# Kernel optimization log

Measured on AMD Instinct MI355X. Metric: run time of the kernel, lower is better.

The kernel has to match this reference:

```python
import jax, jax.numpy as jnp
import numpy as np

N_HEAD = 16
DROP_P = 0.1


def setup_inputs() -> dict:
    key = jax.random.key(0)
    ks = jax.random.split(key, 5)
    B, T, C = 2, 2048, 1024
    return {
        "x": jax.random.normal(ks[0], (B, T, C), dtype=jnp.float32),
        "w_attn": jax.random.normal(ks[1], (C, 3 * C), dtype=jnp.float32) * 0.02,
        "b_attn": jax.random.normal(ks[2], (3 * C,), dtype=jnp.float32) * 0.02,
        "w_proj": jax.random.normal(ks[3], (C, C), dtype=jnp.float32) * 0.02,
        "b_proj": jax.random.normal(ks[4], (C,), dtype=jnp.float32) * 0.02,
    }


def reference(x, w_attn, b_attn, w_proj, b_proj):
    B, T, C = x.shape
    H = N_HEAD
    D = C // H  # head dim
    qkv = x @ w_attn + b_attn                      # [B,T,3C]
    q, k, v = jnp.split(qkv, 3, axis=-1)
    # [B,T,C] -> [B,H,T,D]
    q = q.reshape(B, T, H, D).transpose(0, 2, 1, 3)
    k = k.reshape(B, T, H, D).transpose(0, 2, 1, 3)
    v = v.reshape(B, T, H, D).transpose(0, 2, 1, 3)
    scale = 1.0 / jnp.sqrt(jnp.float32(D))
    attn = jnp.einsum("bhqd,bhkd->bhqk", q, k) * scale  # [B,H,T,T]
    causal = jnp.tril(jnp.ones((T, T), dtype=bool))
    attn = jnp.where(causal[None, None], attn, jnp.float32(-jnp.inf))
    attn = jax.nn.softmax(attn, axis=-1)
    # dropout p=0.1 (training mode in original); deterministic fixed key here
    keep = jax.random.bernoulli(jax.random.key(42), 1.0 - DROP_P, attn.shape)
    attn = jnp.where(keep, attn / (1.0 - DROP_P), 0.0)
    out = jnp.einsum("bhqk,bhkd->bhqd", attn, v)   # [B,H,T,D]
    out = out.transpose(0, 2, 1, 3).reshape(B, T, C)
    return out @ w_proj + b_proj
```

## Files before the change

### kernel.cpp

```cpp
#include <hip/hip_runtime.h>
#include <hip/hip_bf16.h>
#include <stdint.h>
#include <math.h>

#define TSEQ   2048
#define NBATCH 2
#define NHEAD  16
#define HDIM   64
#define CDIM   1024

#define KEEP_LIMIT 3865470464u
#define QSC 0.18033688011112042f

typedef short  bf16x8 __attribute__((ext_vector_type(8)));
typedef float  f32x4  __attribute__((ext_vector_type(4)));

__device__ __forceinline__ float fast_exp2(float x) {
    float r; asm("v_exp_f32 %0, %1" : "=v"(r) : "v"(x)); return r;
}
__device__ __forceinline__ uint32_t cvt_pk_bf16(float a, float b) {
    uint32_t r; asm("v_cvt_pk_bf16_f32 %0, %1, %2" : "=v"(r) : "v"(a), "v"(b)); return r;
}

__device__ __forceinline__ uint32_t rotl32(uint32_t x, int r) {
    return __builtin_amdgcn_alignbit(x, x, 32 - r);
}

__device__ __forceinline__ uint32_t tf2x32_xor(uint32_t x0, uint32_t x1) {
    const uint32_t ka = 0u, kb = 42u;
    const uint32_t kc = ka ^ kb ^ 0x1BD11BDAu;
    x0 += ka; x1 += kb;
#define TFR(r) { x0 += x1; x1 = rotl32(x1, r); x1 ^= x0; }
    TFR(13) TFR(15) TFR(26) TFR(6)
    x0 += kb; x1 += kc + 1u;
    TFR(17) TFR(29) TFR(16) TFR(24)
    x0 += kc; x1 += ka + 2u;
    TFR(13) TFR(15) TFR(26) TFR(6)
    x0 += ka; x1 += kb + 3u;
    TFR(17) TFR(29) TFR(16) TFR(24)
    x0 += kb; x1 += kc + 4u;
    TFR(13) TFR(15) TFR(26) TFR(6)
    x0 += kc; x1 += ka + 5u;
#undef TFR
    return x0 ^ x1;
}

__device__ __forceinline__ float bf2f(ushort u) {
    union { uint32_t i; float f; } c; c.i = ((uint32_t)u) << 16; return c.f;
}

__device__ __forceinline__ void async_copy16(void* lds, const void* g) {
    __builtin_amdgcn_global_load_lds(
        (const __attribute__((address_space(1))) unsigned int*)g,
        (__attribute__((address_space(3))) unsigned int*)lds, 16, 0, 0);
}

__global__ __launch_bounds__(256) void prep(
    const float* __restrict__ x, ushort* __restrict__ xb,
    const float* __restrict__ wA, ushort* __restrict__ wTa,
    const float* __restrict__ wP, ushort* __restrict__ wTp)
{
    __shared__ float t[32][33];
    const int nb = blockIdx.x;
    const int i = threadIdx.x;
    if (nb < 2048) {
        int idx = (nb * 256 + i) * 8;
        float4 a = *(const float4*)(x + idx);
        float4 b = *(const float4*)(x + idx + 4);
        uint4 o;
        o.x = cvt_pk_bf16(a.x, a.y); o.y = cvt_pk_bf16(a.z, a.w);
        o.z = cvt_pk_bf16(b.x, b.y); o.w = cvt_pk_bf16(b.z, b.w);
        *(uint4*)(xb + idx) = o;
        return;
    }
    const float* src; ushort* dst; int n0, k0, N, K;
    if (nb < 5120) {
        int tt = nb - 2048;  src = wA; dst = wTa;
        n0 = (tt % 96) * 32; k0 = (tt / 96) * 32; N = 3072; K = 1024;
    } else {
        int tt = nb - 5120;  src = wP; dst = wTp;
        n0 = (tt & 31) * 32; k0 = (tt >> 5) * 32; N = 1024; K = 1024;
    }
    {
        int k = i >> 3, n4 = (i & 7) * 4;
        float4 v = *(const float4*)(src + (size_t)(k0 + k) * N + n0 + n4);
        t[k][n4 + 0] = v.x; t[k][n4 + 1] = v.y; t[k][n4 + 2] = v.z; t[k][n4 + 3] = v.w;
    }
    __syncthreads();
    {
        int n = i >> 3, k4 = (i & 7) * 4;
        uint2 o;
        o.x = cvt_pk_bf16(t[k4 + 0][n], t[k4 + 1][n]);
        o.y = cvt_pk_bf16(t[k4 + 2][n], t[k4 + 3][n]);
        *(uint2*)(dst + (size_t)(n0 + n) * K + k0 + k4) = o;
    }
}

__global__ __launch_bounds__(256) void qkv_mask(
    const ushort* __restrict__ A, const ushort* __restrict__ Bt,
    const float* __restrict__ bias,
    ushort* __restrict__ Q, ushort* __restrict__ Kq, ushort* __restrict__ V,
    unsigned long long* __restrict__ mask)
{
    __shared__ ushort As[2][128 * 32];
    __shared__ ushort Bs[2][128 * 32];
    const int tid = threadIdx.x, lane = tid & 63, wid = tid >> 6;

    if (blockIdx.x >= 768) {
        const int mb   = blockIdx.x - 768;
        const int hb   = mb >> 6;
        const int rem  = mb & 63;
        const int pair = rem >> 2;
        const int quad = rem & 3;
        const int lim  = (pair + 1) << 6;
        const int base = quad * 528 + wid * 132;
#pragma unroll 1
        for (int it = 0; it < 33; ++it) {
            uint32_t idxs[4], qrow[4]; int kts[4];
#pragma unroll
            for (int j = 0; j < 4; ++j) {
                const int u = base + it * 4 + j;
                const bool first = (u < lim);
                const int qt = first ? pair : 31 - pair;
                const int uu = first ? u : u - lim;
                const int kt = uu >> 6, q = uu & 63;
                qrow[j] = ((uint32_t)hb << 11) + (uint32_t)((qt << 6) + q);
                idxs[j] = qrow[j] * 2048u + (uint32_t)(kt << 6) + (uint32_t)lane;
                kts[j] = kt;
            }
            uint32_t bits[4];
#pragma unroll
            for (int j = 0; j < 4; ++j) bits[j] = tf2x32_xor(0u, idxs[j]);
#pragma unroll
            for (int j = 0; j < 4; ++j) {
                const unsigned long long bal = __ballot(bits[j] < KEEP_LIMIT);
                if (lane == j)
                    mask[((size_t)qrow[j] << 5) + kts[j]] = bal;
            }
        }
        return;
    }

    const int l15 = lane & 15, l4 = lane >> 4;
    const int wr = wid >> 1, wc = wid & 1;
    const int bn = blockIdx.x % 24, bm = blockIdx.x / 24;
    const int K = 1024, NTK = K >> 5;

    f32x4 acc[4][4];
#pragma unroll
    for (int m = 0; m < 4; ++m)
#pragma unroll
        for (int n = 0; n < 4; ++n) acc[m][n] = (f32x4){0.f, 0.f, 0.f, 0.f};

    auto stage = [&](int p, int k0) {
#pragma unroll
        for (int j = 0; j < 2; ++j) {
            const int rbase = wid * 32 + j * 16;
            const int row = rbase + (lane >> 2);
            const ushort* src = A + (size_t)(bm * 128 + row) * K + k0 + (lane & 3) * 8;
            async_copy16(&As[p][rbase * 32], src);
        }
#pragma unroll
        for (int j = 0; j < 2; ++j) {
            const int rbase = wid * 32 + j * 16;
            const int row = rbase + (lane >> 2);
            const ushort* src = Bt + (size_t)(bn * 128 + row) * K + k0 + (lane & 3) * 8;
            async_copy16(&Bs[p][rbase * 32], src);
        }
    };
    auto compute = [&](int p) {
        bf16x8 af[4], bf[4];
#pragma unroll
        for (int m = 0; m < 4; ++m)
            af[m] = *(const bf16x8*)&As[p][(wr * 64 + m * 16 + l15) * 32 + l4 * 8];
#pragma unroll
        for (int n = 0; n < 4; ++n)
            bf[n] = *(const bf16x8*)&Bs[p][(wc * 64 + n * 16 + l15) * 32 + l4 * 8];
#pragma unroll
        for (int m = 0; m < 4; ++m)
#pragma unroll
            for (int n = 0; n < 4; ++n)
                acc[m][n] = __builtin_amdgcn_mfma_f32_16x16x32_bf16(af[m], bf[n], acc[m][n], 0, 0, 0);
    };

    stage(0, 0);
    __syncthreads();
    for (int t = 0; t < NTK; ++t) {
        const int p = t & 1;
        if (t + 1 < NTK) stage(p ^ 1, (t + 1) << 5);
        compute(p);
        __syncthreads();
    }

    const int colbase = bn * 128 + wc * 64;
    const int rowbase = bm * 128 + wr * 64;
#pragma unroll
    for (int n = 0; n < 4; ++n) {
        const int col = colbase + n * 16 + l15;
        const int which = col >> 10, cc = col & 1023;
        const int hh = cc >> 6, dd = cc & 63;
        const float bv = bias[col];
        const float sc = (which == 0) ? QSC : 1.0f;
#pragma unroll
        for (int m = 0; m < 4; ++m) {
            float v0 = (acc[m][n][0] + bv) * sc, v1 = (acc[m][n][1] + bv) * sc;
            float v2 = (acc[m][n][2] + bv) * sc, v3 = (acc[m][n][3] + bv) * sc;
            uint32_t pk01 = cvt_pk_bf16(v0, v1), pk23 = cvt_pk_bf16(v2, v3);
            ushort vals[4] = { (ushort)pk01, (ushort)(pk01 >> 16),
                               (ushort)pk23, (ushort)(pk23 >> 16) };
#pragma unroll
            for (int r = 0; r < 4; ++r) {
                const int row = rowbase + m * 16 + l4 * 4 + r;
                const int bb = row >> 11, tt = row & 2047;
                if (which == 0)
                    Q[(((size_t)(bb * NHEAD + hh)) * TSEQ + tt) * HDIM + dd] = vals[r];
                else if (which == 1)
                    Kq[(((size_t)(bb * NHEAD + hh)) * TSEQ + tt) * HDIM + dd] = vals[r];
                else
                    V[(((size_t)(bb * NHEAD + hh)) * HDIM + dd) * TSEQ + tt] = vals[r];
            }
        }
    }
}

__global__ __launch_bounds__(256) void proj_gemm(
    const ushort* __restrict__ A, const ushort* __restrict__ Bt,
    const float* __restrict__ bias, float* __restrict__ Cf, int M, int N, int K)
{
    __shared__ ushort As[2][128 * 32];
    __shared__ ushort Bs[2][128 * 32];
    const int tid = threadIdx.x, lane = tid & 63, wid = tid >> 6;
    const int l15 = lane & 15, l4 = lane >> 4;
    const int wr = wid >> 1, wc = wid & 1;
    const int bn = blockIdx.x, bm = blockIdx.y;
    const int NTK = K >> 5;

    f32x4 acc[4][4];
#pragma unroll
    for (int m = 0; m < 4; ++m)
#pragma unroll
        for (int n = 0; n < 4; ++n) acc[m][n] = (f32x4){0.f, 0.f, 0.f, 0.f};

    auto stage = [&](int p, int k0) {
#pragma unroll
        for (int j = 0; j < 2; ++j) {
            const int rbase = wid * 32 + j * 16;
            const int row = rbase + (lane >> 2);
            const ushort* src = A + (size_t)(bm * 128 + row) * K + k0 + (lane & 3) * 8;
            async_copy16(&As[p][rbase * 32], src);
        }
#pragma unroll
        for (int j = 0; j < 2; ++j) {
            const int rbase = wid * 32 + j * 16;
            const int row = rbase + (lane >> 2);
            const ushort* src = Bt + (size_t)(bn * 128 + row) * K + k0 + (lane & 3) * 8;
            async_copy16(&Bs[p][rbase * 32], src);
        }
    };
    auto compute = [&](int p) {
        bf16x8 af[4], bf[4];
#pragma unroll
        for (int m = 0; m < 4; ++m)
            af[m] = *(const bf16x8*)&As[p][(wr * 64 + m * 16 + l15) * 32 + l4 * 8];
#pragma unroll
        for (int n = 0; n < 4; ++n)
            bf[n] = *(const bf16x8*)&Bs[p][(wc * 64 + n * 16 + l15) * 32 + l4 * 8];
#pragma unroll
        for (int m = 0; m < 4; ++m)
#pragma unroll
            for (int n = 0; n < 4; ++n)
                acc[m][n] = __builtin_amdgcn_mfma_f32_16x16x32_bf16(af[m], bf[n], acc[m][n], 0, 0, 0);
    };

    stage(0, 0);
    __syncthreads();
    for (int t = 0; t < NTK; ++t) {
        const int p = t & 1;
        if (t + 1 < NTK) stage(p ^ 1, (t + 1) << 5);
        compute(p);
        __syncthreads();
    }

    const int colbase = bn * 128 + wc * 64;
    const int rowbase = bm * 128 + wr * 64;
#pragma unroll
    for (int n = 0; n < 4; ++n) {
        const int col = colbase + n * 16 + l15;
        const float bv = bias[col];
#pragma unroll
        for (int m = 0; m < 4; ++m)
#pragma unroll
            for (int r = 0; r < 4; ++r) {
                const int row = rowbase + m * 16 + l4 * 4 + r;
                Cf[(size_t)row * N + col] = acc[m][n][r] + bv;
            }
    }
}

__global__ __launch_bounds__(256) void attn_fwd_mfma(
    const ushort* __restrict__ Qb, const ushort* __restrict__ Kb,
    const ushort* __restrict__ VbT, const unsigned long long* __restrict__ Mk,
    ushort* __restrict__ Ap, float* __restrict__ lp)
{
    __shared__ ushort Ks[64 * 64];
    __shared__ ushort Vt[2][64 * 64];
    __shared__ ushort Ps[64 * 64];
    const int tid = threadIdx.x;
    const int lane = tid & 63;
    const int wid = tid >> 6;
    const int l15 = lane & 15, l4 = lane >> 4;
    const int pair = blockIdx.x >> 1, half = blockIdx.x & 1;
    const int h = blockIdx.y, b = blockIdx.z;
    const int hb = b * NHEAD + h;
    const size_t headoff = (size_t)hb * TSEQ * HDIM;
    const ushort* Qg = Qb + headoff;
    const ushort* Kg = Kb + headoff;
    const ushort* Vg = VbT + headoff;

    auto stageK = [&](int kt) {
        const ushort* Kt = Kg + (size_t)(kt * 64) * HDIM;
#pragma unroll
        for (int c = 0; c < 2; ++c) {
            const int rbase = wid * 16 + c * 8;
            const int row = rbase + (lane >> 3);
            const ushort* srcK = Kt + row * 64 + (((lane & 7) * 8) ^ ((row & 7) << 3));
            async_copy16(&Ks[rbase * 64], srcK);
        }
    };
    auto stageV = [&](int p, int kt) {
        const ushort* Vt0 = Vg + kt * 64;
#pragma unroll
        for (int c = 0; c < 2; ++c) {
            const int rbase = wid * 16 + c * 8;
            const int row = rbase + (lane >> 3);
            const ushort* srcV = Vt0 + (size_t)row * TSEQ + (((lane & 7) * 8) ^ ((row & 7) << 3));
            async_copy16(&Vt[p][rbase * 64], srcV);
        }
    };

    const int swq = (l15 & 7) << 3;
    const int prow = wid * 16 + l15;

    for (int pass = 0; pass < 2; ++pass) {
        const int qt = pass ? (TSEQ / 64 - 1) - pair : pair;
        const int ntk = qt + 1;
        const int kb = half ? (ntk + 1) >> 1 : 0;
        const int ke = half ? ntk : (ntk + 1) >> 1;
        const int pidx = (hb * 32 + qt) * 2 + half;
        const int tilerow = wid * 16 + l15;
        ushort* arow = Ap + (size_t)pidx * 4096 + tilerow * 64;

        if (kb >= ke) {
#pragma unroll
            for (int dt = 0; dt < 4; ++dt) {
                ushort4 z; z.x = z.y = z.z = z.w = 0;
                *(ushort4*)&arow[dt * 16 + l4 * 4] = z;
            }
            if (l4 == 0) lp[pidx * 64 + tilerow] = 0.f;
            continue;
        }

        const int qglob = qt * 64 + tilerow;
        const unsigned long long* mrow = Mk + ((size_t)(hb * TSEQ + qglob) << 5);
        bf16x8 qf0, qf1;
        {
            const ushort* qrow = Qg + (size_t)qglob * HDIM;
            qf0 = *(const bf16x8*)(qrow + l4 * 8);
            qf1 = *(const bf16x8*)(qrow + 32 + l4 * 8);
        }

        f32x4 oacc[4];
#pragma unroll
        for (int i = 0; i < 4; ++i) oacc[i] = (f32x4){0.f, 0.f, 0.f, 0.f};
        float li = 0.f;

        stageK(kb);
        stageV(0, kb);
        __syncthreads();

        for (int kt = kb; kt < ke; ++kt) {
            const int p = (kt - kb) & 1;
            const bool hasNext = (kt + 1 < ke);
            if (hasNext) stageV(p ^ 1, kt + 1);

            const unsigned long long m64 = mrow[kt];

            f32x4 s4[4];
#pragma unroll
            for (int ct = 0; ct < 4; ++ct) {
                const int krow = ct * 16 + l15;
                const int sw = (krow & 7) << 3;
                bf16x8 kf0 = *(const bf16x8*)&Ks[krow * 64 + ((l4 * 8) ^ sw)];
                bf16x8 kf1 = *(const bf16x8*)&Ks[krow * 64 + ((l4 * 8 + 32) ^ sw)];
                f32x4 a = {0.f, 0.f, 0.f, 0.f};
                a = __builtin_amdgcn_mfma_f32_16x16x32_bf16(kf0, qf0, a, 0, 0, 0);
                a = __builtin_amdgcn_mfma_f32_16x16x32_bf16(kf1, qf1, a, 0, 0, 0);
                s4[ct] = a;
            }
            __syncthreads();
            if (hasNext) stageK(kt + 1);

            const int kb0 = kt * 64;
            if (kt == qt) {
#pragma unroll
                for (int ct = 0; ct < 4; ++ct)
#pragma unroll
                    for (int r = 0; r < 4; ++r) {
                        const int kglob = kb0 + ct * 16 + l4 * 4 + r;
                        s4[ct][r] = (kglob <= qglob) ? s4[ct][r] : -INFINITY;
                    }
            }
            float rs = 0.f;
#pragma unroll
            for (int ct = 0; ct < 4; ++ct)
#pragma unroll
                for (int r = 0; r < 4; ++r) {
                    s4[ct][r] = fast_exp2(s4[ct][r]);
                    rs += s4[ct][r];
                }
            li += rs;

#pragma unroll
            for (int ct = 0; ct < 4; ++ct) {
                const uint32_t nib = (uint32_t)(m64 >> (ct * 16 + l4 * 4)) & 0xFu;
                const float p0 = (nib & 1u) ? s4[ct][0] : 0.f;
                const float p1 = (nib & 2u) ? s4[ct][1] : 0.f;
                const float p2 = (nib & 4u) ? s4[ct][2] : 0.f;
                const float p3 = (nib & 8u) ? s4[ct][3] : 0.f;
                uint2 pk;
                pk.x = cvt_pk_bf16(p0, p1);
                pk.y = cvt_pk_bf16(p2, p3);
                *(uint2*)&Ps[prow * 64 + ((ct * 16 + l4 * 4) ^ swq)] = pk;
            }

            bf16x8 pf0 = *(const bf16x8*)&Ps[prow * 64 + ((l4 * 8) ^ swq)];
            bf16x8 pf1 = *(const bf16x8*)&Ps[prow * 64 + ((l4 * 8 + 32) ^ swq)];
#pragma unroll
            for (int dt = 0; dt < 4; ++dt) {
                const int drow = dt * 16 + l15;
                const int swv = (drow & 7) << 3;
                bf16x8 vf0 = *(const bf16x8*)&Vt[p][drow * 64 + ((l4 * 8) ^ swv)];
                bf16x8 vf1 = *(const bf16x8*)&Vt[p][drow * 64 + ((l4 * 8 + 32) ^ swv)];
                oacc[dt] = __builtin_amdgcn_mfma_f32_16x16x32_bf16(vf0, pf0, oacc[dt], 0, 0, 0);
                oacc[dt] = __builtin_amdgcn_mfma_f32_16x16x32_bf16(vf1, pf1, oacc[dt], 0, 0, 0);
            }
            __syncthreads();
        }

#pragma unroll
        for (int dt = 0; dt < 4; ++dt) {
            uint2 o;
            o.x = cvt_pk_bf16(oacc[dt][0], oacc[dt][1]);
            o.y = cvt_pk_bf16(oacc[dt][2], oacc[dt][3]);
            *(uint2*)&arow[dt * 16 + l4 * 4] = o;
        }
        float rs = li;
        rs += __shfl_xor(rs, 16);
        rs += __shfl_xor(rs, 32);
        if (l4 == 0) lp[pidx * 64 + tilerow] = rs;
    }
}

__global__ __launch_bounds__(256) void attn_merge(
    const ushort* __restrict__ Ap, const float* __restrict__ lp,
    ushort* __restrict__ AO)
{
    const int gidx = blockIdx.x * 16 + (threadIdx.x >> 4);
    const int hb = gidx >> 11;
    const int q  = gidx & 2047;
    const int qt = q >> 6, row = q & 63;
    const int sub = (threadIdx.x & 15) * 4;
    const int pidx0 = (hb * 32 + qt) * 2;
    const int pr = pidx0 * 64 + row;
    const float l0 = lp[pr], l1 = lp[pr + 64];
    const float inv = 1.0f / ((l0 + l1) * 0.9f);
    ushort4 a0 = *(const ushort4*)&Ap[(size_t)pidx0 * 4096 + row * 64 + sub];
    ushort4 a1 = *(const ushort4*)&Ap[(size_t)(pidx0 + 1) * 4096 + row * 64 + sub];
    const int b = hb >> 4, h = hb & 15;
    ushort* orow = AO + ((size_t)(b * TSEQ + q)) * CDIM + h * HDIM + sub;
    uint2 o;
    o.x = cvt_pk_bf16((bf2f(a0.x) + bf2f(a1.x)) * inv,
                      (bf2f(a0.y) + bf2f(a1.y)) * inv);
    o.y = cvt_pk_bf16((bf2f(a0.z) + bf2f(a1.z)) * inv,
                      (bf2f(a0.w) + bf2f(a1.w)) * inv);
    *(uint2*)orow = o;
}

extern "C" void kernel_launch(void* const* d_in, const int* in_sizes, int n_in,
                              void* d_out, int out_size, void* d_ws, size_t ws_size,
                              hipStream_t stream)
{
    const float* x      = (const float*)d_in[0];
    const float* w_attn = (const float*)d_in[1];
    const float* b_attn = (const float*)d_in[2];
    const float* w_proj = (const float*)d_in[3];
    const float* b_proj = (const float*)d_in[4];
    float* out = (float*)d_out;

    const size_t NH = (size_t)NBATCH * NHEAD * TSEQ * HDIM;
    ushort* Qb  = (ushort*)d_ws;
    ushort* Kb  = Qb + NH;
    ushort* VbT = Kb + NH;
    ushort* AO  = VbT + NH;
    ushort* xb  = AO + NH;
    ushort* wTa = xb + NH;
    ushort* wTp = wTa + (size_t)3072 * 1024;
    unsigned long long* Mk = (unsigned long long*)(wTp + (size_t)1024 * 1024);
    float*  lp  = (float*)(Mk + (size_t)65536 * 32);

    ushort* Aparts = (ushort*)d_out;

    prep<<<6144, 256, 0, stream>>>(x, xb, w_attn, wTa, w_proj, wTp);

    qkv_mask<<<768 + 2048, 256, 0, stream>>>(
        xb, wTa, b_attn, Qb, Kb, VbT, Mk);

    attn_fwd_mfma<<<dim3(32, NHEAD, NBATCH), 256, 0, stream>>>(
        Qb, Kb, VbT, Mk, Aparts, lp);

    attn_merge<<<4096, 256, 0, stream>>>(Aparts, lp, AO);

    proj_gemm<<<dim3(8, 32), 256, 0, stream>>>(
        AO, wTp, b_proj, out, 4096, 1024, 1024);
}
```

Before: 268.8 us.

## Generate dropout mask inline in attention kernel instead of precomputing bitmask

Removes the separate mask-generation blocks from the QKV GEMM launch and the global bitmask buffer. The attention kernel now evaluates the threefry hash per score element inside its inner loop. This trades the global mask traffic and the extra mask blocks for 16 threefry evaluations per lane per key tile, which adds ALU work to the attention hot loop.

```diff
diff --git a/kernel.cpp b/kernel.cpp
--- a/kernel.cpp
+++ b/kernel.cpp
@@ -96,54 +96,17 @@
     }
 }
 
-__global__ __launch_bounds__(256) void qkv_mask(
+__global__ __launch_bounds__(256) void qkv_gemm(
     const ushort* __restrict__ A, const ushort* __restrict__ Bt,
     const float* __restrict__ bias,
-    ushort* __restrict__ Q, ushort* __restrict__ Kq, ushort* __restrict__ V,
-    unsigned long long* __restrict__ mask)
+    ushort* __restrict__ Q, ushort* __restrict__ Kq, ushort* __restrict__ V)
 {
     __shared__ ushort As[2][128 * 32];
     __shared__ ushort Bs[2][128 * 32];
     const int tid = threadIdx.x, lane = tid & 63, wid = tid >> 6;
-
-    if (blockIdx.x >= 768) {
-        const int mb   = blockIdx.x - 768;
-        const int hb   = mb >> 6;
-        const int rem  = mb & 63;
-        const int pair = rem >> 2;
-        const int quad = rem & 3;
-        const int lim  = (pair + 1) << 6;
-        const int base = quad * 528 + wid * 132;
-#pragma unroll 1
-        for (int it = 0; it < 33; ++it) {
-            uint32_t idxs[4], qrow[4]; int kts[4];
-#pragma unroll
-            for (int j = 0; j < 4; ++j) {
-                const int u = base + it * 4 + j;
-                const bool first = (u < lim);
-                const int qt = first ? pair : 31 - pair;
-                const int uu = first ? u : u - lim;
-                const int kt = uu >> 6, q = uu & 63;
-                qrow[j] = ((uint32_t)hb << 11) + (uint32_t)((qt << 6) + q);
-                idxs[j] = qrow[j] * 2048u + (uint32_t)(kt << 6) + (uint32_t)lane;
-                kts[j] = kt;
-            }
-            uint32_t bits[4];
-#pragma unroll
-            for (int j = 0; j < 4; ++j) bits[j] = tf2x32_xor(0u, idxs[j]);
-#pragma unroll
-            for (int j = 0; j < 4; ++j) {
-                const unsigned long long bal = __ballot(bits[j] < KEEP_LIMIT);
-                if (lane == j)
-                    mask[((size_t)qrow[j] << 5) + kts[j]] = bal;
-            }
-        }
-        return;
-    }
-
     const int l15 = lane & 15, l4 = lane >> 4;
     const int wr = wid >> 1, wc = wid & 1;
-    const int bn = blockIdx.x % 24, bm = blockIdx.x / 24;
+    const int bn = blockIdx.x, bm = blockIdx.y;
     const int K = 1024, NTK = K >> 5;
 
     f32x4 acc[4][4];
@@ -299,7 +262,7 @@
 
 __global__ __launch_bounds__(256) void attn_fwd_mfma(
     const ushort* __restrict__ Qb, const ushort* __restrict__ Kb,
-    const ushort* __restrict__ VbT, const unsigned long long* __restrict__ Mk,
+    const ushort* __restrict__ VbT,
     ushort* __restrict__ Ap, float* __restrict__ lp)
 {
     __shared__ ushort Ks[64 * 64];
@@ -361,7 +324,6 @@
         }
 
         const int qglob = qt * 64 + tilerow;
-        const unsigned long long* mrow = Mk + ((size_t)(hb * TSEQ + qglob) << 5);
         bf16x8 qf0, qf1;
         {
             const ushort* qrow = Qg + (size_t)qglob * HDIM;
@@ -373,6 +335,7 @@
 #pragma unroll
         for (int i = 0; i < 4; ++i) oacc[i] = (f32x4){0.f, 0.f, 0.f, 0.f};
         float li = 0.f;
+        const uint32_t rowbase = ((uint32_t)hb * TSEQ + (uint32_t)qglob) * TSEQ;
 
         stageK(kb);
         stageV(0, kb);
@@ -383,7 +346,17 @@
             const bool hasNext = (kt + 1 < ke);
             if (hasNext) stageV(p ^ 1, kt + 1);
 
-            const unsigned long long m64 = mrow[kt];
+            const int kb0 = kt * 64;
+            const uint32_t idx0 = rowbase + (uint32_t)kb0 + (uint32_t)(l4 * 4);
+            uint32_t tfb[4][4];
+#pragma unroll
+            for (int ct = 0; ct < 4; ++ct) {
+                const uint32_t kk = idx0 + (uint32_t)(ct * 16);
+                tfb[ct][0] = tf2x32_xor(0u, kk + 0u);
+                tfb[ct][1] = tf2x32_xor(0u, kk + 1u);
+                tfb[ct][2] = tf2x32_xor(0u, kk + 2u);
+                tfb[ct][3] = tf2x32_xor(0u, kk + 3u);
+            }
 
             f32x4 s4[4];
 #pragma unroll
@@ -400,7 +373,6 @@
             __syncthreads();
             if (hasNext) stageK(kt + 1);
 
-            const int kb0 = kt * 64;
             if (kt == qt) {
 #pragma unroll
                 for (int ct = 0; ct < 4; ++ct)
@@ -422,11 +394,10 @@
 
 #pragma unroll
             for (int ct = 0; ct < 4; ++ct) {
-                const uint32_t nib = (uint32_t)(m64 >> (ct * 16 + l4 * 4)) & 0xFu;
-                const float p0 = (nib & 1u) ? s4[ct][0] : 0.f;
-                const float p1 = (nib & 2u) ? s4[ct][1] : 0.f;
-                const float p2 = (nib & 4u) ? s4[ct][2] : 0.f;
-                const float p3 = (nib & 8u) ? s4[ct][3] : 0.f;
+                const float p0 = (tfb[ct][0] < KEEP_LIMIT) ? s4[ct][0] : 0.f;
+                const float p1 = (tfb[ct][1] < KEEP_LIMIT) ? s4[ct][1] : 0.f;
+                const float p2 = (tfb[ct][2] < KEEP_LIMIT) ? s4[ct][2] : 0.f;
+                const float p3 = (tfb[ct][3] < KEEP_LIMIT) ? s4[ct][3] : 0.f;
                 uint2 pk;
                 pk.x = cvt_pk_bf16(p0, p1);
                 pk.y = cvt_pk_bf16(p2, p3);
@@ -505,18 +476,17 @@
     ushort* xb  = AO + NH;
     ushort* wTa = xb + NH;
     ushort* wTp = wTa + (size_t)3072 * 1024;
-    unsigned long long* Mk = (unsigned long long*)(wTp + (size_t)1024 * 1024);
-    float*  lp  = (float*)(Mk + (size_t)65536 * 32);
+    float*  lp  = (float*)(wTp + (size_t)1024 * 1024);
 
     ushort* Aparts = (ushort*)d_out;
 
     prep<<<6144, 256, 0, stream>>>(x, xb, w_attn, wTa, w_proj, wTp);
 
-    qkv_mask<<<768 + 2048, 256, 0, stream>>>(
-        xb, wTa, b_attn, Qb, Kb, VbT, Mk);
+    qkv_gemm<<<dim3(24, 32), 256, 0, stream>>>(
+        xb, wTa, b_attn, Qb, Kb, VbT);
 
     attn_fwd_mfma<<<dim3(32, NHEAD, NBATCH), 256, 0, stream>>>(
-        Qb, Kb, VbT, Mk, Aparts, lp);
+        Qb, Kb, VbT, Aparts, lp);
 
     attn_merge<<<4096, 256, 0, stream>>>(Aparts, lp, AO);
 
```

After: 232.0 us. 13.7% less time.
